# Kernel tuning notes

Measured on AMD Instinct MI355X. Metric: run time of the kernel, lower is better.

The kernel has to match this reference:

```python
import jax, jax.numpy as jnp
import numpy as np
import math

B, S, D, H = 4, 1024, 1024, 16
DK = D // H
DF = 4 * D
SPARSITY = 0.3
EPS = 1e-5

def _ln(x, g, b):
    mu = jnp.mean(x, axis=-1, keepdims=True)
    var = jnp.mean((x - mu) ** 2, axis=-1, keepdims=True)
    return (x - mu) * jax.lax.rsqrt(var + EPS) * g + b

def setup_inputs() -> dict:
    key = jax.random.key(0)
    ks = jax.random.split(key, 8)
    sc = 0.02
    return {
        "x": jax.random.normal(ks[0], (B, S, D), jnp.float32),
        "Wq": jax.random.normal(ks[1], (D, D), jnp.float32) * sc,
        "bq": jnp.zeros((D,), jnp.float32),
        "Wk": jax.random.normal(ks[2], (D, D), jnp.float32) * sc,
        "bk": jnp.zeros((D,), jnp.float32),
        "Wv": jax.random.normal(ks[3], (D, D), jnp.float32) * sc,
        "bv": jnp.zeros((D,), jnp.float32),
        "Wo": jax.random.normal(ks[4], (D, D), jnp.float32) * sc,
        "bo": jnp.zeros((D,), jnp.float32),
        "W1": jax.random.normal(ks[5], (DF, D), jnp.float32) * sc,
        "b1": jnp.zeros((DF,), jnp.float32),
        "Wm": jax.random.normal(ks[6], (DF, DF), jnp.float32) * sc,
        "bm": jnp.zeros((DF,), jnp.float32),
        "W2": jax.random.normal(ks[7], (D, DF), jnp.float32) * sc,
        "b2": jnp.zeros((D,), jnp.float32),
        "g1": jnp.ones((D,), jnp.float32),
        "be1": jnp.zeros((D,), jnp.float32),
        "g2": jnp.ones((D,), jnp.float32),
        "be2": jnp.zeros((D,), jnp.float32),
    }

def reference(x, Wq, bq, Wk, bk, Wv, bv, Wo, bo, W1, b1, Wm, bm, W2, b2, g1, be1, g2, be2):
    h = _ln(x, g1, be1)
    def heads(W, b):
        return (h @ W.T + b).reshape(B, S, H, DK).transpose(0, 2, 1, 3)  # [B,H,S,DK]
    Q, K, V = heads(Wq, bq), heads(Wk, bk), heads(Wv, bv)
    scores = jnp.einsum("bhqd,bhkd->bhqk", Q, K) / math.sqrt(DK)  # [B,H,S,S]
    k = max(1, int(S * SPARSITY))
    vals, idx = jax.lax.top_k(scores, k)  # [B,H,S,k]
    # scatter top-k values into a -inf canvas (faithful to torch scatter_)
    N = B * H * S
    rows = jnp.arange(N)[:, None]
    mask2 = jnp.full((N, S), -jnp.inf, scores.dtype)
    mask2 = mask2.at[rows, idx.reshape(N, k)].set(vals.reshape(N, k))
    attn = jax.nn.softmax(mask2.reshape(B, H, S, S), axis=-1)
    out = jnp.einsum("bhqk,bhkd->bhqd", attn, V)
    out = out.transpose(0, 2, 1, 3).reshape(B, S, D) @ Wo.T + bo
    x = x + out
    h2 = _ln(x, g2, be2)
    f = jax.nn.gelu(h2 @ W1.T + b1, approximate=False)
    f = jax.nn.gelu(f @ Wm.T + bm, approximate=False)
    f = f @ W2.T + b2
    x = x + f
    return x, attn
```

## Files before the change

kernel.cpp:

```cpp
#include <hip/hip_runtime.h>
#include <hip/hip_bf16.h>

typedef __hip_bfloat16 bf16;
typedef float v4f __attribute__((ext_vector_type(4)));
typedef short v8s __attribute__((ext_vector_type(8)));

#define KSEL 307

__device__ static inline void async16(bf16* lds, const bf16* g) {
    __builtin_amdgcn_global_load_lds(
        (const __attribute__((address_space(1))) void*)g,
        (__attribute__((address_space(3))) void*)lds, 16, 0, 0);
}

__device__ static inline unsigned short f2bu(float f) {
    __hip_bfloat16 h = __float2bfloat16(f);
    return *reinterpret_cast<unsigned short*>(&h);
}

__device__ static inline unsigned pk2(float a, float b) {
    __hip_bfloat162 h = __float22bfloat162_rn(make_float2(a, b));
    return *reinterpret_cast<unsigned*>(&h);
}

__device__ static inline float gelu_f(float v) {
    float c = v * fmaf(v * v, 0.0356774081f, 0.7978845608f);
    return v / (1.0f + __expf(-2.0f * c));
}

struct F2BP { const float* src[7]; bf16* dst[7]; int n4[7]; };

__global__ void __launch_bounds__(256) f2b_multi(F2BP p) {
    int s = blockIdx.y;
    const float* __restrict__ in = p.src[s];
    bf16* __restrict__ out = p.dst[s];
    int n4 = p.n4[s];
    for (int i = blockIdx.x * 256 + threadIdx.x; i < n4; i += gridDim.x * 256) {
        float4 v = ((const float4*)in)[i];
        ushort4 u = make_ushort4(f2bu(v.x), f2bu(v.y), f2bu(v.z), f2bu(v.w));
        ((ushort4*)out)[i] = u;
    }
}

__global__ void __launch_bounds__(256) ln_kernel(const float* __restrict__ x,
                                                 const float* __restrict__ g,
                                                 const float* __restrict__ be,
                                                 bf16* __restrict__ out) {
    int row = blockIdx.x;
    int tid = threadIdx.x;
    const float* xr = x + row * 1024;
    float4 v = ((const float4*)xr)[tid];
    float s = v.x + v.y + v.z + v.w;
    float s2 = v.x*v.x + v.y*v.y + v.z*v.z + v.w*v.w;
    for (int off = 32; off > 0; off >>= 1) {
        s  += __shfl_down(s, off);
        s2 += __shfl_down(s2, off);
    }
    __shared__ float sh[4], sh2[4];
    int w = tid >> 6;
    if ((tid & 63) == 0) { sh[w] = s; sh2[w] = s2; }
    __syncthreads();
    float mean = (sh[0]+sh[1]+sh[2]+sh[3]) * (1.0f / 1024.f);
    float ms   = (sh2[0]+sh2[1]+sh2[2]+sh2[3]) * (1.0f / 1024.f);
    float var  = ms - mean*mean;
    float rs   = rsqrtf(var + 1e-5f);
    float4 gg = ((const float4*)g)[tid];
    float4 bb = ((const float4*)be)[tid];
    ushort4 o = make_ushort4(
        f2bu((v.x-mean)*rs*gg.x + bb.x),
        f2bu((v.y-mean)*rs*gg.y + bb.y),
        f2bu((v.z-mean)*rs*gg.z + bb.z),
        f2bu((v.w-mean)*rs*gg.w + bb.w));
    ((ushort4*)out)[row * 256 + tid] = o;
}

__global__ void __launch_bounds__(256) topk_softmax(const unsigned short* __restrict__ scb,
                                                    float* __restrict__ out) {
    __shared__ int hist[4][256];
    const int tid = threadIdx.x;
    const int wid = tid >> 6, lane = tid & 63;
    const long long row = (long long)blockIdx.x * 4 + wid;
    const unsigned short* pb = scb + row * 1024;
    float* po = out + row * 1024;
    int* h = hist[wid];

    unsigned short raw[16];
    unsigned key[16];
    float v[16];
#pragma unroll
    for (int j = 0; j < 4; ++j) {
        ushort4 t = *(const ushort4*)(pb + lane * 4 + j * 256);
        raw[j*4+0] = t.x; raw[j*4+1] = t.y; raw[j*4+2] = t.z; raw[j*4+3] = t.w;
    }
#pragma unroll
    for (int j = 0; j < 16; ++j) {
        unsigned u = raw[j];
        key[j] = (u & 0x8000u) ? (0xFFFFu & ~u) : (u | 0x8000u);
        v[j] = __uint_as_float(u << 16);
    }

    unsigned prefix = 0;
    int need = KSEL;
#pragma unroll
    for (int pass = 0; pass < 2; ++pass) {
        const int shift = 8 - 8 * pass;
        *(int4*)&h[lane * 4] = make_int4(0, 0, 0, 0);
        asm volatile("s_waitcnt lgkmcnt(0)" ::: "memory");
#pragma unroll
        for (int j = 0; j < 16; ++j) {
            bool cand = (pass == 0) || ((key[j] >> 8) == prefix);
            if (cand) atomicAdd(&h[(key[j] >> shift) & 255], 1);
        }
        asm volatile("s_waitcnt lgkmcnt(0)" ::: "memory");
        int4 hc = *(const int4*)&h[lane * 4];
        int s_local = hc.x + hc.y + hc.z + hc.w;
        int sfx = s_local;
#pragma unroll
        for (int off = 1; off < 64; off <<= 1) {
            int o = __shfl_down(sfx, off);
            if (lane + off < 64) sfx += o;
        }
        int sfx_next = __shfl_down(sfx, 1);
        if (lane == 63) sfx_next = 0;
        int above_lane = sfx - s_local;
        int suf3 = above_lane + hc.w;
        int suf2 = suf3 + hc.z;
        int suf1 = suf2 + hc.y;
        int suf0 = suf1 + hc.x;
        int bloc = -1, abv = 0;
        if (suf0 >= need && suf1 < need)     { bloc = lane*4+0; abv = suf1; }
        if (suf1 >= need && suf2 < need)     { bloc = lane*4+1; abv = suf2; }
        if (suf2 >= need && suf3 < need)     { bloc = lane*4+2; abv = suf3; }
        if (suf3 >= need && sfx_next < need) { bloc = lane*4+3; abv = sfx_next; }
        unsigned long long mask = __ballot(bloc >= 0);
        int src = __ffsll((unsigned long long)mask) - 1;
        int b = __shfl(bloc, src);
        int above = __shfl(abv, src);
        prefix = (prefix << 8) | (unsigned)b;
        need -= above;
    }

    float mx = v[0];
#pragma unroll
    for (int j = 1; j < 16; ++j) mx = fmaxf(mx, v[j]);
#pragma unroll
    for (int off = 32; off > 0; off >>= 1) mx = fmaxf(mx, __shfl_xor(mx, off));
    float sum = 0.f;
#pragma unroll
    for (int j = 0; j < 16; ++j) {
        bool sel = key[j] >= prefix;
        v[j] = sel ? __expf(v[j] - mx) : 0.f;
        sum += v[j];
    }
#pragma unroll
    for (int off = 32; off > 0; off >>= 1) sum += __shfl_xor(sum, off);
    float inv = 1.0f / sum;
#pragma unroll
    for (int j = 0; j < 4; ++j) {
        float4 o;
        o.x = v[j*4+0]*inv; o.y = v[j*4+1]*inv; o.z = v[j*4+2]*inv; o.w = v[j*4+3]*inv;
        *(float4*)(po + lane * 4 + j * 256) = o;
    }
}

template<int K, int LDA, int LDB, int LDC, int N, int BMODE, int ACT, int BM>
__global__ void __launch_bounds__(256) gemm_t(const bf16* __restrict__ A,
                                              const bf16* __restrict__ B,
                                              float* __restrict__ Cf,
                                              bf16* __restrict__ Cb,
                                              const float* __restrict__ bias,
                                              const float* __restrict__ resid,
                                              float scale) {
    __shared__ __align__(16) bf16 As[128 * 32];
    __shared__ __align__(16) bf16 Bs[128 * 32];
    int offA = 0, offB = 0, offC = 0;
    if (BM == 1) {
        int z = blockIdx.z;
        int b = z >> 4, h = z & 15;
        offA = b * 1048576 + h * 64;
        offB = offA;
        offC = z * 1048576;
    }
    const int tid = threadIdx.x;
    const int w = tid >> 6, lane = tid & 63;
    const int tm = blockIdx.y * 128, tn = blockIdx.x * 128;
    const int q = lane >> 4, m16 = lane & 15;
    const int r0 = (w >> 1) * 64, c0 = (w & 1) * 64;
    const int srow = lane >> 2;
    const int scol = ((lane & 3) ^ ((lane >> 3) & 3)) * 8;
    const int sq = q ^ ((m16 >> 1) & 3);

    v4f acc[4][4];
#pragma unroll
    for (int i = 0; i < 4; ++i)
#pragma unroll
        for (int j = 0; j < 4; ++j) acc[i][j] = (v4f){0.f, 0.f, 0.f, 0.f};

    const bf16* Ab = A + offA + (tm + w * 16 + srow) * LDA + scol;
    const bf16* Bb = B + offB + (tn + w * 16 + srow) * LDB + scol;
    bf16* Asw = &As[(w * 16) * 32];
    bf16* Bsw = &Bs[(w * 16) * 32];

#pragma unroll 1
    for (int k0 = 0; k0 < K; k0 += 32) {
        async16(Asw,           Ab + k0);
        async16(Asw + 64 * 32, Ab + 64 * LDA + k0);
        async16(Bsw,           Bb + k0);
        async16(Bsw + 64 * 32, Bb + 64 * LDB + k0);
        __syncthreads();
        v8s af[4], bfr[4];
#pragma unroll
        for (int i = 0; i < 4; ++i)
            af[i] = *(const v8s*)&As[(r0 + 16 * i + m16) * 32 + sq * 8];
#pragma unroll
        for (int j = 0; j < 4; ++j)
            bfr[j] = *(const v8s*)&Bs[(c0 + 16 * j + m16) * 32 + sq * 8];
#pragma unroll
        for (int i = 0; i < 4; ++i)
#pragma unroll
            for (int j = 0; j < 4; ++j)
                acc[i][j] = __builtin_amdgcn_mfma_f32_16x16x32_bf16(af[i], bfr[j], acc[i][j], 0, 0, 0);
        __syncthreads();
    }

    float bc[4];
#pragma unroll
    for (int j = 0; j < 4; ++j)
        bc[j] = (BMODE == 1) ? bias[tn + c0 + 16 * j + m16] : 0.f;

#pragma unroll
    for (int i = 0; i < 4; ++i) {
#pragma unroll
        for (int r = 0; r < 4; ++r) {
            int row = tm + r0 + 16 * i + q * 4 + r;
            float br = (BMODE == 2) ? bias[row] : 0.f;
            int rowbase = offC + row * LDC + tn + c0 + m16;
#pragma unroll
            for (int j = 0; j < 4; ++j) {
                float v = acc[i][j][r] * scale + bc[j] + br;
                if (ACT) v = gelu_f(v);
                int idx = rowbase + 16 * j;
                if (resid) v += resid[idx];
                if (Cf) Cf[idx] = v;
                if (Cb) Cb[idx] = __float2bfloat16(v);
            }
        }
    }
}

template<int K, int LDA, int LDB, int LDC>
__global__ void __launch_bounds__(512, 2) gemm256(const bf16* __restrict__ A,
                                                  const bf16* __restrict__ B,
                                                  bf16* __restrict__ C,
                                                  const float* __restrict__ bias) {
    __shared__ __align__(16) bf16 As[4][256 * 32];
    __shared__ __align__(16) bf16 Bs[4][256 * 32];

    constexpr int nt = K / 32;
    static_assert(nt >= 4 && (nt % 4) == 0, "K must be multiple of 128");

    const int tid = threadIdx.x;
    const int w = tid >> 6, lane = tid & 63;
    const int wm = w >> 2, wn = w & 3;
    const int q = lane >> 4, m16 = lane & 15;

    int bid = blockIdx.y * 16 + blockIdx.x;
    int xcd = bid & 7, inner = bid >> 3;
    int by = (xcd & 3) * 4 + (inner & 3);
    int bx = (xcd >> 2) * 8 + (inner >> 2);
    const int tm = by * 256, tn = bx * 256;

    const int srow = lane >> 2;
    const int scol = ((lane & 3) ^ ((lane >> 3) & 3)) * 8;
    const bf16* Ag = A + (tm + w * 32 + srow) * LDA + scol;
    const bf16* Bg = B + (tn + w * 32 + srow) * LDB + scol;

    v4f acc[8][4];
#pragma unroll
    for (int i = 0; i < 8; ++i)
#pragma unroll
        for (int j = 0; j < 4; ++j) acc[i][j] = (v4f){0.f, 0.f, 0.f, 0.f};

    const int sq = q ^ ((m16 >> 1) & 3);
    const int aoff = (wm * 128 + m16) * 32 + sq * 8;
    const int boff = (wn * 64 + m16) * 32 + sq * 8;

#pragma unroll
    for (int t = 0; t < 2; ++t) {
        async16(&As[t][(w * 32) * 32],      Ag + t * 32);
        async16(&As[t][(w * 32 + 16) * 32], Ag + 16 * LDA + t * 32);
        async16(&Bs[t][(w * 32) * 32],      Bg + t * 32);
        async16(&Bs[t][(w * 32 + 16) * 32], Bg + 16 * LDB + t * 32);
    }
    asm volatile("s_waitcnt vmcnt(4)" ::: "memory");
    __builtin_amdgcn_s_barrier();
    __builtin_amdgcn_sched_barrier(0);

#pragma unroll 1
    for (int t4 = 0; t4 < nt; t4 += 4) {
#pragma unroll
        for (int tt = 0; tt < 4; ++tt) {
            const int t = t4 + tt;
            const int cur = tt;
            const int pre = (tt + 2) & 3;
            int kt = t + 2; if (kt >= nt) kt = 0;
            const bf16* Asrc = Ag + kt * 32;
            const bf16* Bsrc = Bg + kt * 32;

            v8s af[4], bfr[4];
#pragma unroll
            for (int i = 0; i < 4; ++i)
                af[i] = *(const v8s*)&As[cur][aoff + i * 512];
#pragma unroll
            for (int j = 0; j < 4; ++j)
                bfr[j] = *(const v8s*)&Bs[cur][boff + j * 512];
            async16(&As[pre][(w * 32) * 32],      Asrc);
            async16(&As[pre][(w * 32 + 16) * 32], Asrc + 16 * LDA);
            __builtin_amdgcn_s_barrier();
            asm volatile("s_waitcnt lgkmcnt(0)" ::: "memory");
            __builtin_amdgcn_sched_barrier(0);
            __builtin_amdgcn_s_setprio(1);
#pragma unroll
            for (int i = 0; i < 4; ++i)
#pragma unroll
                for (int j = 0; j < 4; ++j)
                    acc[i][j] = __builtin_amdgcn_mfma_f32_16x16x32_bf16(af[i], bfr[j], acc[i][j], 0, 0, 0);
            __builtin_amdgcn_s_setprio(0);
            __builtin_amdgcn_sched_barrier(0);
            __builtin_amdgcn_s_barrier();
            __builtin_amdgcn_sched_barrier(0);

            v8s af2[4];
#pragma unroll
            for (int i = 0; i < 4; ++i)
                af2[i] = *(const v8s*)&As[cur][aoff + 2048 + i * 512];
            async16(&Bs[pre][(w * 32) * 32],      Bsrc);
            async16(&Bs[pre][(w * 32 + 16) * 32], Bsrc + 16 * LDB);
            __builtin_amdgcn_s_barrier();
            asm volatile("s_waitcnt lgkmcnt(0)" ::: "memory");
            __builtin_amdgcn_sched_barrier(0);
            __builtin_amdgcn_s_setprio(1);
#pragma unroll
            for (int i = 0; i < 4; ++i)
#pragma unroll
                for (int j = 0; j < 4; ++j)
                    acc[i + 4][j] = __builtin_amdgcn_mfma_f32_16x16x32_bf16(af2[i], bfr[j], acc[i + 4][j], 0, 0, 0);
            __builtin_amdgcn_s_setprio(0);
            asm volatile("s_waitcnt vmcnt(4)" ::: "memory");
            __builtin_amdgcn_sched_barrier(0);
            __builtin_amdgcn_s_barrier();
            __builtin_amdgcn_sched_barrier(0);
        }
    }

    float bc[4];
#pragma unroll
    for (int j = 0; j < 4; ++j)
        bc[j] = bias[tn + wn * 64 + 16 * j + m16];

#pragma unroll
    for (int i = 0; i < 8; ++i) {
#pragma unroll
        for (int r = 0; r < 4; ++r) {
            int row = tm + wm * 128 + 16 * i + q * 4 + r;
            int rowbase = row * LDC + tn + wn * 64 + m16;
#pragma unroll
            for (int j = 0; j < 4; ++j) {
                float v = acc[i][j][r] + bc[j];
                v = gelu_f(v);
                C[rowbase + 16 * j] = __float2bfloat16(v);
            }
        }
    }
}

__global__ void __launch_bounds__(256) attnv_kernel(const float* __restrict__ P,
                                                    const bf16* __restrict__ VT,
                                                    bf16* __restrict__ out) {
    __shared__ __align__(16) bf16 As[128 * 32];
    __shared__ __align__(16) bf16 Bs[64 * 32];
    int z = blockIdx.z, b = z >> 4, h = z & 15;
    int tid = threadIdx.x, w = tid >> 6, lane = tid & 63;
    int q = lane >> 4, m16 = lane & 15;
    int srow = lane >> 2, scol = (lane & 3) * 8;

    const float* Ab = P + z * 1048576 + (blockIdx.y * 128 + (tid >> 1)) * 1024 + (tid & 1) * 16;
    const bf16* Bb = VT + (h * 64 + w * 16 + srow) * 4096 + b * 1024 + scol;
    uint4* asd = (uint4*)&As[(tid >> 1) * 32 + (tid & 1) * 16];
    bf16* bsw = &Bs[(w * 16) * 32];

    v4f acc[2][4];
#pragma unroll
    for (int i = 0; i < 2; ++i)
#pragma unroll
        for (int j = 0; j < 4; ++j) acc[i][j] = (v4f){0.f, 0.f, 0.f, 0.f};

#pragma unroll 1
    for (int k0 = 0; k0 < 1024; k0 += 32) {
        const float4* s4 = (const float4*)(Ab + k0);
        float4 f0 = s4[0], f1 = s4[1], f2 = s4[2], f3 = s4[3];
        async16(bsw, Bb + k0);
        uint4 u0, u1;
        u0.x = pk2(f0.x, f0.y); u0.y = pk2(f0.z, f0.w);
        u0.z = pk2(f1.x, f1.y); u0.w = pk2(f1.z, f1.w);
        u1.x = pk2(f2.x, f2.y); u1.y = pk2(f2.z, f2.w);
        u1.z = pk2(f3.x, f3.y); u1.w = pk2(f3.z, f3.w);
        asd[0] = u0; asd[1] = u1;
        __syncthreads();
        v8s af[2], bfr[4];
        af[0] = *(const v8s*)&As[(w * 32 + m16) * 32 + q * 8];
        af[1] = *(const v8s*)&As[(w * 32 + 16 + m16) * 32 + q * 8];
#pragma unroll
        for (int j = 0; j < 4; ++j)
            bfr[j] = *(const v8s*)&Bs[(16 * j + m16) * 32 + q * 8];
#pragma unroll
        for (int i = 0; i < 2; ++i)
#pragma unroll
            for (int j = 0; j < 4; ++j)
                acc[i][j] = __builtin_amdgcn_mfma_f32_16x16x32_bf16(af[i], bfr[j], acc[i][j], 0, 0, 0);
        __syncthreads();
    }

    int orow0 = b * 1024 + blockIdx.y * 128 + w * 32;
#pragma unroll
    for (int i = 0; i < 2; ++i)
#pragma unroll
        for (int r = 0; r < 4; ++r) {
            int row = orow0 + 16 * i + q * 4 + r;
#pragma unroll
            for (int j = 0; j < 4; ++j) {
                int col = h * 64 + 16 * j + m16;
                out[row * 1024 + col] = __float2bfloat16(acc[i][j][r]);
            }
        }
}

extern "C" void kernel_launch(void* const* d_in, const int* in_sizes, int n_in,
                              void* d_out, int out_size, void* d_ws, size_t ws_size,
                              hipStream_t stream) {
    (void)in_sizes; (void)n_in; (void)out_size; (void)ws_size;
    const float* x  = (const float*)d_in[0];
    const float* Wq = (const float*)d_in[1];
    const float* bq = (const float*)d_in[2];
    const float* Wk = (const float*)d_in[3];
    const float* bk = (const float*)d_in[4];
    const float* Wv = (const float*)d_in[5];
    const float* bv = (const float*)d_in[6];
    const float* Wo = (const float*)d_in[7];
    const float* bo = (const float*)d_in[8];
    const float* W1 = (const float*)d_in[9];
    const float* b1 = (const float*)d_in[10];
    const float* Wm = (const float*)d_in[11];
    const float* bm = (const float*)d_in[12];
    const float* W2 = (const float*)d_in[13];
    const float* b2 = (const float*)d_in[14];
    const float* g1 = (const float*)d_in[15];
    const float* be1 = (const float*)d_in[16];
    const float* g2 = (const float*)d_in[17];
    const float* be2 = (const float*)d_in[18];

    char* ws = (char*)d_ws;
    const size_t MB = 1024 * 1024;
    bf16* WQb = (bf16*)(ws + 0 * MB);
    bf16* WKb = (bf16*)(ws + 2 * MB);
    bf16* WVb = (bf16*)(ws + 4 * MB);
    bf16* WOb = (bf16*)(ws + 6 * MB);
    bf16* W1b = (bf16*)(ws + 8 * MB);
    bf16* WMb = (bf16*)(ws + 16 * MB);
    bf16* W2b = (bf16*)(ws + 48 * MB);
    bf16* HB  = (bf16*)(ws + 56 * MB);
    bf16* QB  = (bf16*)(ws + 64 * MB);
    bf16* KB  = (bf16*)(ws + 72 * MB);
    bf16* VT  = (bf16*)(ws + 80 * MB);
    bf16* AT  = (bf16*)(ws + 88 * MB);
    float* X1 = (float*)(ws + 96 * MB);
    bf16* F1  = (bf16*)(ws + 112 * MB);
    bf16* F2  = (bf16*)(ws + 144 * MB);
    bf16* SCb = (bf16*)(ws + 96 * MB);

    float* out_x  = (float*)d_out;
    float* scores = out_x + 4194304;

    F2BP fp;
    fp.src[0] = Wq; fp.dst[0] = WQb; fp.n4[0] = 262144;
    fp.src[1] = Wk; fp.dst[1] = WKb; fp.n4[1] = 262144;
    fp.src[2] = Wv; fp.dst[2] = WVb; fp.n4[2] = 262144;
    fp.src[3] = Wo; fp.dst[3] = WOb; fp.n4[3] = 262144;
    fp.src[4] = W1; fp.dst[4] = W1b; fp.n4[4] = 1048576;
    fp.src[5] = Wm; fp.dst[5] = WMb; fp.n4[5] = 4194304;
    fp.src[6] = W2; fp.dst[6] = W2b; fp.n4[6] = 1048576;
    hipLaunchKernelGGL(f2b_multi, dim3(1024, 7), dim3(256), 0, stream, fp);

    hipLaunchKernelGGL(ln_kernel, dim3(4096), dim3(256), 0, stream, x, g1, be1, HB);

    gemm_t<1024,1024,1024,1024,1024,1,0,0><<<dim3(8,32,1), 256, 0, stream>>>(
        HB, WQb, nullptr, QB, bq, nullptr, 1.f);
    gemm_t<1024,1024,1024,1024,1024,1,0,0><<<dim3(8,32,1), 256, 0, stream>>>(
        HB, WKb, nullptr, KB, bk, nullptr, 1.f);
    gemm_t<1024,1024,1024,4096,4096,2,0,0><<<dim3(32,8,1), 256, 0, stream>>>(
        WVb, HB, nullptr, VT, bv, nullptr, 1.f);

    gemm_t<64,1024,1024,1024,1024,0,0,1><<<dim3(8,8,64), 256, 0, stream>>>(
        QB, KB, nullptr, SCb, nullptr, nullptr, 0.125f);

    hipLaunchKernelGGL(topk_softmax, dim3(16384), dim3(256), 0, stream,
                       (const unsigned short*)SCb, scores);

    hipLaunchKernelGGL(attnv_kernel, dim3(1,8,64), dim3(256), 0, stream, scores, VT, AT);

    gemm_t<1024,1024,1024,1024,1024,1,0,0><<<dim3(8,32,1), 256, 0, stream>>>(
        AT, WOb, X1, nullptr, bo, x, 1.f);

    hipLaunchKernelGGL(ln_kernel, dim3(4096), dim3(256), 0, stream, X1, g2, be2, HB);

    gemm256<1024,1024,1024,4096><<<dim3(16,16,1), 512, 0, stream>>>(HB, W1b, F1, b1);
    gemm256<4096,4096,4096,4096><<<dim3(16,16,1), 512, 0, stream>>>(F1, WMb, F2, bm);

    gemm_t<4096,4096,4096,1024,1024,1,0,0><<<dim3(8,32,1), 256, 0, stream>>>(
        F2, W2b, out_x, nullptr, b2, X1, 1.f);
}
```

Baseline: 1.058 ms.

## Add pipelined 128x128 GEMM and feed attention-V from a bf16 probability copy

Adds gemm128p, a 512-thread 128x128 tile GEMM with a 4-stage async global-to-LDS ring buffer, swizzled LDS layout, prefetch two tiles ahead and one barrier per step. It replaces gemm_t for the Q/K/V, output-projection and W2 GEMMs. The top-k softmax kernel now also writes bf16 probabilities over the score buffer, so attnv reads half as many bytes through the same async pipelined load path instead of converting fp32 to bf16 in registers. The cost is an extra bf16 store per softmax row and more LDS per block, which may lower occupancy.

```diff
diff --git a/kernel.cpp b/kernel.cpp
--- a/kernel.cpp
+++ b/kernel.cpp
@@ -74,13 +74,13 @@
     ((ushort4*)out)[row * 256 + tid] = o;
 }
 
-__global__ void __launch_bounds__(256) topk_softmax(const unsigned short* __restrict__ scb,
+__global__ void __launch_bounds__(256) topk_softmax(unsigned short* __restrict__ scb,
                                                     float* __restrict__ out) {
     __shared__ int hist[4][256];
     const int tid = threadIdx.x;
     const int wid = tid >> 6, lane = tid & 63;
     const long long row = (long long)blockIdx.x * 4 + wid;
-    const unsigned short* pb = scb + row * 1024;
+    unsigned short* pb = scb + row * 1024;
     float* po = out + row * 1024;
     int* h = hist[wid];
 
@@ -160,6 +160,9 @@
         float4 o;
         o.x = v[j*4+0]*inv; o.y = v[j*4+1]*inv; o.z = v[j*4+2]*inv; o.w = v[j*4+3]*inv;
         *(float4*)(po + lane * 4 + j * 256) = o;
+        uint2 u;
+        u.x = pk2(o.x, o.y); u.y = pk2(o.z, o.w);
+        *(uint2*)(pb + lane * 4 + j * 256) = u;
     }
 }
 
@@ -248,6 +251,103 @@
     }
 }
 
+template<int K, int LDA, int LDB, int LDC, int BMODE>
+__global__ void __launch_bounds__(512, 2) gemm128p(const bf16* __restrict__ A,
+                                                   const bf16* __restrict__ B,
+                                                   float* __restrict__ Cf,
+                                                   bf16* __restrict__ Cb,
+                                                   const float* __restrict__ bias,
+                                                   const float* __restrict__ resid) {
+    __shared__ __align__(16) bf16 As[4][128 * 32];
+    __shared__ __align__(16) bf16 Bs[4][128 * 32];
+
+    constexpr int nt = K / 32;
+    static_assert(nt >= 4, "K >= 128");
+
+    const int tid = threadIdx.x;
+    const int w = tid >> 6, lane = tid & 63;
+    const int wr = w >> 2, wc = w & 3;
+    const int q = lane >> 4, m16 = lane & 15;
+    const int tm = blockIdx.y * 128, tn = blockIdx.x * 128;
+
+    const int srow = lane >> 2;
+    const int scol = ((lane & 3) ^ ((lane >> 3) & 3)) * 8;
+    const bf16* Ag = A + (tm + w * 16 + srow) * LDA + scol;
+    const bf16* Bg = B + (tn + w * 16 + srow) * LDB + scol;
+
+    v4f acc[4][2];
+#pragma unroll
+    for (int i = 0; i < 4; ++i)
+#pragma unroll
+        for (int j = 0; j < 2; ++j) acc[i][j] = (v4f){0.f, 0.f, 0.f, 0.f};
+
+    const int sq = q ^ ((m16 >> 1) & 3);
+    const int aoff = (wr * 64 + m16) * 32 + sq * 8;
+    const int boff = (wc * 32 + m16) * 32 + sq * 8;
+
+#pragma unroll
+    for (int t = 0; t < 2; ++t) {
+        async16(&As[t][(w * 16) * 32], Ag + t * 32);
+        async16(&Bs[t][(w * 16) * 32], Bg + t * 32);
+    }
+    asm volatile("s_waitcnt vmcnt(2)" ::: "memory");
+    __builtin_amdgcn_s_barrier();
+    __builtin_amdgcn_sched_barrier(0);
+
+#pragma unroll 1
+    for (int t = 0; t < nt; ++t) {
+        const int cur = t & 3, pre = (t + 2) & 3;
+        const int kt = (t + 2 < nt) ? (t + 2) : 0;
+        v8s af[4], bfr[2];
+#pragma unroll
+        for (int i = 0; i < 4; ++i)
+            af[i] = *(const v8s*)&As[cur][aoff + i * 512];
+#pragma unroll
+        for (int j = 0; j < 2; ++j)
+            bfr[j] = *(const v8s*)&Bs[cur][boff + j * 512];
+        async16(&As[pre][(w * 16) * 32], Ag + kt * 32);
+        async16(&Bs[pre][(w * 16) * 32], Bg + kt * 32);
+        asm volatile("s_waitcnt lgkmcnt(0)" ::: "memory");
+        __builtin_amdgcn_sched_barrier(0);
+        __builtin_amdgcn_s_setprio(1);
+#pragma unroll
+        for (int i = 0; i < 4; ++i)
+#pragma unroll
+            for (int j = 0; j < 2; ++j)
+                acc[i][j] = __builtin_amdgcn_mfma_f32_16x16x32_bf16(af[i], bfr[j], acc[i][j], 0, 0, 0);
+        __builtin_amdgcn_s_setprio(0);
+        __builtin_amdgcn_sched_barrier(0);
+        asm volatile("s_waitcnt vmcnt(2)" ::: "memory");
+        __builtin_amdgcn_sched_barrier(0);
+        __builtin_amdgcn_s_barrier();
+        __builtin_amdgcn_sched_barrier(0);
+    }
+    asm volatile("s_waitcnt vmcnt(0)" ::: "memory");
+
+    float bc[2];
+#pragma unroll
+    for (int j = 0; j < 2; ++j)
+        bc[j] = (BMODE == 1) ? bias[tn + wc * 32 + 16 * j + m16] : 0.f;
+
+#pragma unroll
+    for (int i = 0; i < 4; ++i) {
+#pragma unroll
+        for (int r = 0; r < 4; ++r) {
+            int row = tm + wr * 64 + 16 * i + q * 4 + r;
+            float br = (BMODE == 2) ? bias[row] : 0.f;
+            int rowbase = row * LDC + tn + wc * 32 + m16;
+#pragma unroll
+            for (int j = 0; j < 2; ++j) {
+                float v = acc[i][j][r] + bc[j] + br;
+                int idx = rowbase + 16 * j;
+                if (resid) v += resid[idx];
+                if (Cf) Cf[idx] = v;
+                if (Cb) Cb[idx] = __float2bfloat16(v);
+            }
+        }
+    }
+}
+
 template<int K, int LDA, int LDB, int LDC>
 __global__ void __launch_bounds__(512, 2) gemm256(const bf16* __restrict__ A,
                                                   const bf16* __restrict__ B,
@@ -374,20 +474,20 @@
     }
 }
 
-__global__ void __launch_bounds__(256) attnv_kernel(const float* __restrict__ P,
+__global__ void __launch_bounds__(256) attnv_kernel(const bf16* __restrict__ P,
                                                     const bf16* __restrict__ VT,
                                                     bf16* __restrict__ out) {
-    __shared__ __align__(16) bf16 As[128 * 32];
-    __shared__ __align__(16) bf16 Bs[64 * 32];
+    __shared__ __align__(16) bf16 As[4][128 * 32];
+    __shared__ __align__(16) bf16 Bs[4][64 * 32];
     int z = blockIdx.z, b = z >> 4, h = z & 15;
     int tid = threadIdx.x, w = tid >> 6, lane = tid & 63;
     int q = lane >> 4, m16 = lane & 15;
-    int srow = lane >> 2, scol = (lane & 3) * 8;
-
-    const float* Ab = P + z * 1048576 + (blockIdx.y * 128 + (tid >> 1)) * 1024 + (tid & 1) * 16;
+    int srow = lane >> 2;
+    int scol = ((lane & 3) ^ ((lane >> 3) & 3)) * 8;
+    const int sq = q ^ ((m16 >> 1) & 3);
+
+    const bf16* Ab = P + z * 1048576 + (blockIdx.y * 128 + w * 16 + srow) * 1024 + scol;
     const bf16* Bb = VT + (h * 64 + w * 16 + srow) * 4096 + b * 1024 + scol;
-    uint4* asd = (uint4*)&As[(tid >> 1) * 32 + (tid & 1) * 16];
-    bf16* bsw = &Bs[(w * 16) * 32];
 
     v4f acc[2][4];
 #pragma unroll
@@ -395,31 +495,48 @@
 #pragma unroll
         for (int j = 0; j < 4; ++j) acc[i][j] = (v4f){0.f, 0.f, 0.f, 0.f};
 
+    const int aoff = (w * 32 + m16) * 32 + sq * 8;
+    const int boff = (m16) * 32 + sq * 8;
+
+#pragma unroll
+    for (int t = 0; t < 2; ++t) {
+        async16(&As[t][(w * 16) * 32],        Ab + t * 32);
+        async16(&As[t][(64 + w * 16) * 32],   Ab + 64 * 1024 + t * 32);
+        async16(&Bs[t][(w * 16) * 32],        Bb + t * 32);
+    }
+    asm volatile("s_waitcnt vmcnt(3)" ::: "memory");
+    __builtin_amdgcn_s_barrier();
+    __builtin_amdgcn_sched_barrier(0);
+
 #pragma unroll 1
-    for (int k0 = 0; k0 < 1024; k0 += 32) {
-        const float4* s4 = (const float4*)(Ab + k0);
-        float4 f0 = s4[0], f1 = s4[1], f2 = s4[2], f3 = s4[3];
-        async16(bsw, Bb + k0);
-        uint4 u0, u1;
-        u0.x = pk2(f0.x, f0.y); u0.y = pk2(f0.z, f0.w);
-        u0.z = pk2(f1.x, f1.y); u0.w = pk2(f1.z, f1.w);
-        u1.x = pk2(f2.x, f2.y); u1.y = pk2(f2.z, f2.w);
-        u1.z = pk2(f3.x, f3.y); u1.w = pk2(f3.z, f3.w);
-        asd[0] = u0; asd[1] = u1;
-        __syncthreads();
+    for (int t = 0; t < 32; ++t) {
+        const int cur = t & 3, pre = (t + 2) & 3;
+        const int kt = (t + 2 < 32) ? (t + 2) : 0;
         v8s af[2], bfr[4];
-        af[0] = *(const v8s*)&As[(w * 32 + m16) * 32 + q * 8];
-        af[1] = *(const v8s*)&As[(w * 32 + 16 + m16) * 32 + q * 8];
+        af[0] = *(const v8s*)&As[cur][aoff];
+        af[1] = *(const v8s*)&As[cur][aoff + 512];
 #pragma unroll
         for (int j = 0; j < 4; ++j)
-            bfr[j] = *(const v8s*)&Bs[(16 * j + m16) * 32 + q * 8];
+            bfr[j] = *(const v8s*)&Bs[cur][boff + j * 512];
+        async16(&As[pre][(w * 16) * 32],      Ab + kt * 32);
+        async16(&As[pre][(64 + w * 16) * 32], Ab + 64 * 1024 + kt * 32);
+        async16(&Bs[pre][(w * 16) * 32],      Bb + kt * 32);
+        asm volatile("s_waitcnt lgkmcnt(0)" ::: "memory");
+        __builtin_amdgcn_sched_barrier(0);
+        __builtin_amdgcn_s_setprio(1);
 #pragma unroll
         for (int i = 0; i < 2; ++i)
 #pragma unroll
             for (int j = 0; j < 4; ++j)
                 acc[i][j] = __builtin_amdgcn_mfma_f32_16x16x32_bf16(af[i], bfr[j], acc[i][j], 0, 0, 0);
-        __syncthreads();
-    }
+        __builtin_amdgcn_s_setprio(0);
+        __builtin_amdgcn_sched_barrier(0);
+        asm volatile("s_waitcnt vmcnt(3)" ::: "memory");
+        __builtin_amdgcn_sched_barrier(0);
+        __builtin_amdgcn_s_barrier();
+        __builtin_amdgcn_sched_barrier(0);
+    }
+    asm volatile("s_waitcnt vmcnt(0)" ::: "memory");
 
     int orow0 = b * 1024 + blockIdx.y * 128 + w * 32;
 #pragma unroll
@@ -493,29 +610,30 @@
 
     hipLaunchKernelGGL(ln_kernel, dim3(4096), dim3(256), 0, stream, x, g1, be1, HB);
 
-    gemm_t<1024,1024,1024,1024,1024,1,0,0><<<dim3(8,32,1), 256, 0, stream>>>(
-        HB, WQb, nullptr, QB, bq, nullptr, 1.f);
-    gemm_t<1024,1024,1024,1024,1024,1,0,0><<<dim3(8,32,1), 256, 0, stream>>>(
-        HB, WKb, nullptr, KB, bk, nullptr, 1.f);
-    gemm_t<1024,1024,1024,4096,4096,2,0,0><<<dim3(32,8,1), 256, 0, stream>>>(
-        WVb, HB, nullptr, VT, bv, nullptr, 1.f);
+    gemm128p<1024,1024,1024,1024,1><<<dim3(8,32,1), 512, 0, stream>>>(
+        HB, WQb, nullptr, QB, bq, nullptr);
+    gemm128p<1024,1024,1024,1024,1><<<dim3(8,32,1), 512, 0, stream>>>(
+        HB, WKb, nullptr, KB, bk, nullptr);
+    gemm128p<1024,1024,1024,4096,2><<<dim3(32,8,1), 512, 0, stream>>>(
+        WVb, HB, nullptr, VT, bv, nullptr);
 
     gemm_t<64,1024,1024,1024,1024,0,0,1><<<dim3(8,8,64), 256, 0, stream>>>(
         QB, KB, nullptr, SCb, nullptr, nullptr, 0.125f);
 
     hipLaunchKernelGGL(topk_softmax, dim3(16384), dim3(256), 0, stream,
-                       (const unsigned short*)SCb, scores);
-
-    hipLaunchKernelGGL(attnv_kernel, dim3(1,8,64), dim3(256), 0, stream, scores, VT, AT);
-
-    gemm_t<1024,1024,1024,1024,1024,1,0,0><<<dim3(8,32,1), 256, 0, stream>>>(
-        AT, WOb, X1, nullptr, bo, x, 1.f);
+                       (unsigned short*)SCb, scores);
+
+    hipLaunchKernelGGL(attnv_kernel, dim3(1,8,64), dim3(256), 0, stream,
+                       SCb, VT, AT);
+
+    gemm128p<1024,1024,1024,1024,1><<<dim3(8,32,1), 512, 0, stream>>>(
+        AT, WOb, X1, nullptr, bo, x);
 
     hipLaunchKernelGGL(ln_kernel, dim3(4096), dim3(256), 0, stream, X1, g2, be2, HB);
 
     gemm256<1024,1024,1024,4096><<<dim3(16,16,1), 512, 0, stream>>>(HB, W1b, F1, b1);
     gemm256<4096,4096,4096,4096><<<dim3(16,16,1), 512, 0, stream>>>(F1, WMb, F2, bm);
 
-    gemm_t<4096,4096,4096,1024,1024,1,0,0><<<dim3(8,32,1), 256, 0, stream>>>(
-        F2, W2b, out_x, nullptr, b2, X1, 1.f);
-}
+    gemm128p<4096,4096,4096,1024,1><<<dim3(8,32,1), 512, 0, stream>>>(
+        F2, W2b, out_x, nullptr, b2, X1);
+}
```

New measurement: 914.1 us. -13.6%, faster.
